# Optimization experiments

Hardware: AMD Instinct MI355X
Metric: run time of the kernel (lower is better)

The kernel has to match this reference:

```python
import jax, jax.numpy as jnp
import numpy as np

V, H, HALF, L, B = 32000, 512, 256, 1024, 64
LN_EPS = 1e-5
DELTA_EPS = 1e-6


def _forward(seq, embed, ff_w1, ff_b1, ff_w2, ff_b2, ln_g, ln_b,
             sem_w, sem_b, epi_w, epi_b, out_w, out_b):
    # Encoder: embed -> residual FFN -> LayerNorm
    e = embed[seq]                                   # (B, L, H)
    ff = jax.nn.relu(e @ ff_w1 + ff_b1) @ ff_w2 + ff_b2
    x = e + ff
    mu = jnp.mean(x, axis=-1, keepdims=True)
    var = jnp.mean((x - mu) ** 2, axis=-1, keepdims=True)
    h = (x - mu) / jnp.sqrt(var + LN_EPS) * ln_g + ln_b  # (B, L, H)

    # Project all timesteps at once (batched GEMM instead of per-step Linear)
    ks_all = h @ sem_w + sem_b                       # (B, L, half)
    ke_all = h @ epi_w + epi_b                       # (B, L, half)

    Bsz = seq.shape[0]
    Ls = seq.shape[1]
    w_t = jnp.arange(1, Ls, dtype=h.dtype) / Ls      # (L-1,) linear recency weights

    def step(carry, inp):
        M_s, M_e = carry
        k_s, k_e, w = inp                            # (B, half), (B, half), scalar
        vps = jnp.einsum('bij,bj->bi', M_s, k_s)
        dvs = k_s - vps / (jnp.sum(k_s * k_s, axis=-1, keepdims=True) + DELTA_EPS)
        M_s = M_s + dvs[:, :, None] * k_s[:, None, :]
        vpe = jnp.einsum('bij,bj->bi', M_e, k_e)
        dve = k_e - vpe / (jnp.sum(k_e * k_e, axis=-1, keepdims=True) + DELTA_EPS)
        M_e = M_e + w * (dve[:, :, None] * k_e[:, None, :])
        return (M_s, M_e), None

    M0 = jnp.zeros((Bsz, HALF, HALF), dtype=h.dtype)
    xs = (jnp.swapaxes(ks_all[:, :-1], 0, 1),        # (L-1, B, half)
          jnp.swapaxes(ke_all[:, :-1], 0, 1),
          w_t)
    (M_s, M_e), _ = jax.lax.scan(step, (M0, M0), xs)

    cs = jnp.einsum('bij,bj->bi', M_s, ks_all[:, -1])
    ce = jnp.einsum('bij,bj->bi', M_e, ke_all[:, -1])
    return jnp.concatenate([cs, ce], axis=-1) @ out_w + out_b  # (B, V)


def setup_inputs() -> dict:
    key = jax.random.key(0)
    ks = jax.random.split(key, 8)
    n = lambda k, shape, s=0.02: jax.random.normal(k, shape, jnp.float32) * s
    return {
        'seq': jax.random.randint(ks[0], (B, L), 0, V),
        'embed': n(ks[1], (V, H)),
        'ff_w1': n(ks[2], (H, 2 * H)), 'ff_b1': jnp.zeros((2 * H,), jnp.float32),
        'ff_w2': n(ks[3], (2 * H, H)), 'ff_b2': jnp.zeros((H,), jnp.float32),
        'ln_g': jnp.ones((H,), jnp.float32), 'ln_b': jnp.zeros((H,), jnp.float32),
        'sem_w': n(ks[4], (H, HALF)), 'sem_b': jnp.zeros((HALF,), jnp.float32),
        'epi_w': n(ks[5], (H, HALF)), 'epi_b': jnp.zeros((HALF,), jnp.float32),
        'out_w': n(ks[6], (2 * HALF, V)), 'out_b': jnp.zeros((V,), jnp.float32),
    }


def reference(seq, embed, ff_w1, ff_b1, ff_w2, ff_b2, ln_g, ln_b,
              sem_w, sem_b, epi_w, epi_b, out_w, out_b):
    return _forward(seq, embed, ff_w1, ff_b1, ff_w2, ff_b2, ln_g, ln_b,
                    sem_w, sem_b, epi_w, epi_b, out_w, out_b)
```

## Files before the change

kernel.cpp:

```cpp
#include <hip/hip_runtime.h>

typedef unsigned short ushort_t;
typedef unsigned int uint_t;
typedef __attribute__((ext_vector_type(8))) short short8;
typedef __attribute__((ext_vector_type(4))) float f32x4;

static constexpr int V = 32000, H = 512, HALFD = 256, LSEQ = 1024, BB = 64;

__device__ __forceinline__ ushort_t f2bf(float f) {
    uint_t u = __float_as_uint(f);
    u = (u + 0x7FFFu + ((u >> 16) & 1u)) >> 16;
    return (ushort_t)u;
}
__device__ __forceinline__ float bf2f(ushort_t u) {
    return __uint_as_float(((uint_t)u) << 16);
}
__device__ __forceinline__ float bflo(uint_t u) { return __uint_as_float(u << 16); }
__device__ __forceinline__ float bfhi(uint_t u) { return __uint_as_float(u & 0xffff0000u); }
__device__ __forceinline__ float bfres(float v) { return v - bf2f(f2bf(v)); }

__device__ __forceinline__ uint_t dppswap1(uint_t x) {
    return (uint_t)__builtin_amdgcn_mov_dpp((int)x, 0xB1, 0xF, 0xF, true);
}

__device__ __forceinline__ void st_pair4(ushort_t* p0, int pitch, int codd,
                                         float v0, float v1, float v2, float v3) {
    uint_t b0 = f2bf(v0), b1 = f2bf(v1), b2 = f2bf(v2), b3 = f2bf(v3);
    uint_t q0 = dppswap1(b0), q1 = dppswap1(b1), q2 = dppswap1(b2), q3 = dppswap1(b3);
    uint_t wa = codd ? ((uint_t)q2 | ((uint_t)b2 << 16)) : ((uint_t)b0 | ((uint_t)q0 << 16));
    uint_t wb = codd ? ((uint_t)q3 | ((uint_t)b3 << 16)) : ((uint_t)b1 | ((uint_t)q1 << 16));
    *(uint_t*)(p0) = wa;
    *(uint_t*)(p0 + pitch) = wb;
}

__global__ void transpose_cvt(const float* __restrict__ W, ushort_t* __restrict__ Wt,
                              int K, int N) {
    __shared__ float tile[32][33];
    int k0 = blockIdx.y * 32, n0 = blockIdx.x * 32;
    int tx = threadIdx.x & 31, ty = threadIdx.x >> 5;
    #pragma unroll
    for (int i = 0; i < 32; i += 8)
        tile[ty + i][tx] = W[(size_t)(k0 + ty + i) * N + n0 + tx];
    __syncthreads();
    #pragma unroll
    for (int i = 0; i < 32; i += 8)
        Wt[(size_t)(n0 + ty + i) * K + k0 + tx] = f2bf(tile[tx][ty + i]);
}

__global__ __launch_bounds__(256) void gemm_ffn1(
        const int* __restrict__ seqp, const float* __restrict__ embed,
        const ushort_t* __restrict__ Bt, const float* __restrict__ bias,
        ushort_t* __restrict__ Cout, int N, int K) {
    __shared__ __align__(16) ushort_t Al[128][40];
    __shared__ __align__(16) ushort_t Bl[128][40];
    int t = threadIdx.x;
    int m0 = blockIdx.y * 128, n0 = blockIdx.x * 128;
    int lane = t & 63, wid = t >> 6;
    int wm = (wid & 1) * 64, wn = (wid >> 1) * 64;
    int lid = lane & 15, quad = lane >> 4;
    int srow = t >> 2, skq = (t & 3) * 8;

    int tok0 = seqp[m0 + srow];
    int tok1 = seqp[m0 + 64 + srow];
    const float* e0 = embed + (size_t)tok0 * H + skq;
    const float* e1 = embed + (size_t)tok1 * H + skq;

    f32x4 acc[4][4];
    #pragma unroll
    for (int i = 0; i < 4; ++i)
        #pragma unroll
        for (int j = 0; j < 4; ++j)
            acc[i][j] = (f32x4){0.f, 0.f, 0.f, 0.f};

    for (int k0 = 0; k0 < K; k0 += 32) {
        float4 ea0 = *(const float4*)(e0 + k0);
        float4 eb0 = *(const float4*)(e0 + k0 + 4);
        float4 ea1 = *(const float4*)(e1 + k0);
        float4 eb1 = *(const float4*)(e1 + k0 + 4);
        short8 b0 = *(const short8*)(Bt + (size_t)(n0 + srow) * K + k0 + skq);
        short8 b1 = *(const short8*)(Bt + (size_t)(n0 + 64 + srow) * K + k0 + skq);
        short8 s0, s1;
        s0[0] = (short)f2bf(ea0.x); s0[1] = (short)f2bf(ea0.y);
        s0[2] = (short)f2bf(ea0.z); s0[3] = (short)f2bf(ea0.w);
        s0[4] = (short)f2bf(eb0.x); s0[5] = (short)f2bf(eb0.y);
        s0[6] = (short)f2bf(eb0.z); s0[7] = (short)f2bf(eb0.w);
        s1[0] = (short)f2bf(ea1.x); s1[1] = (short)f2bf(ea1.y);
        s1[2] = (short)f2bf(ea1.z); s1[3] = (short)f2bf(ea1.w);
        s1[4] = (short)f2bf(eb1.x); s1[5] = (short)f2bf(eb1.y);
        s1[6] = (short)f2bf(eb1.z); s1[7] = (short)f2bf(eb1.w);
        __syncthreads();
        *(short8*)&Al[srow][skq]      = s0;
        *(short8*)&Al[64 + srow][skq] = s1;
        *(short8*)&Bl[srow][skq]      = b0;
        *(short8*)&Bl[64 + srow][skq] = b1;
        __syncthreads();
        short8 af[4], bfr[4];
        #pragma unroll
        for (int i = 0; i < 4; ++i)
            af[i] = *(const short8*)&Al[wm + i * 16 + lid][quad * 8];
        #pragma unroll
        for (int i = 0; i < 4; ++i)
            bfr[i] = *(const short8*)&Bl[wn + i * 16 + lid][quad * 8];
        #pragma unroll
        for (int mt = 0; mt < 4; ++mt)
            #pragma unroll
            for (int nt = 0; nt < 4; ++nt)
                acc[mt][nt] = __builtin_amdgcn_mfma_f32_16x16x32_bf16(
                    af[mt], bfr[nt], acc[mt][nt], 0, 0, 0);
    }
    #pragma unroll
    for (int mt = 0; mt < 4; ++mt)
        #pragma unroll
        for (int nt = 0; nt < 4; ++nt)
            #pragma unroll
            for (int rg = 0; rg < 4; ++rg) {
                int row = m0 + wm + mt * 16 + quad * 4 + rg;
                int col = n0 + wn + nt * 16 + lid;
                float v = fmaxf(acc[mt][nt][rg] + bias[col], 0.f);
                Cout[(size_t)row * N + col] = f2bf(v);
            }
}

__global__ __launch_bounds__(256) void gemm_ffn2(
        const ushort_t* __restrict__ A, const ushort_t* __restrict__ Bt,
        const float* __restrict__ bias, const int* __restrict__ seqp,
        const float* __restrict__ embed, ushort_t* __restrict__ Cout,
        int N, int K) {
    __shared__ __align__(16) ushort_t Al[128][40];
    __shared__ __align__(16) ushort_t Bl[128][40];
    int t = threadIdx.x;
    int m0 = blockIdx.y * 128, n0 = blockIdx.x * 128;
    int lane = t & 63, wid = t >> 6;
    int wm = (wid & 1) * 64, wn = (wid >> 1) * 64;
    int lid = lane & 15, quad = lane >> 4;
    int srow = t >> 2, skq = (t & 3) * 8;

    f32x4 acc[4][4];
    #pragma unroll
    for (int i = 0; i < 4; ++i)
        #pragma unroll
        for (int j = 0; j < 4; ++j)
            acc[i][j] = (f32x4){0.f, 0.f, 0.f, 0.f};

    for (int k0 = 0; k0 < K; k0 += 32) {
        short8 a0 = *(const short8*)(A + (size_t)(m0 + srow) * K + k0 + skq);
        short8 a1 = *(const short8*)(A + (size_t)(m0 + 64 + srow) * K + k0 + skq);
        short8 b0 = *(const short8*)(Bt + (size_t)(n0 + srow) * K + k0 + skq);
        short8 b1 = *(const short8*)(Bt + (size_t)(n0 + 64 + srow) * K + k0 + skq);
        __syncthreads();
        *(short8*)&Al[srow][skq]      = a0;
        *(short8*)&Al[64 + srow][skq] = a1;
        *(short8*)&Bl[srow][skq]      = b0;
        *(short8*)&Bl[64 + srow][skq] = b1;
        __syncthreads();
        short8 af[4], bfr[4];
        #pragma unroll
        for (int i = 0; i < 4; ++i)
            af[i] = *(const short8*)&Al[wm + i * 16 + lid][quad * 8];
        #pragma unroll
        for (int i = 0; i < 4; ++i)
            bfr[i] = *(const short8*)&Bl[wn + i * 16 + lid][quad * 8];
        #pragma unroll
        for (int mt = 0; mt < 4; ++mt)
            #pragma unroll
            for (int nt = 0; nt < 4; ++nt)
                acc[mt][nt] = __builtin_amdgcn_mfma_f32_16x16x32_bf16(
                    af[mt], bfr[nt], acc[mt][nt], 0, 0, 0);
    }
    #pragma unroll
    for (int mt = 0; mt < 4; ++mt)
        #pragma unroll
        for (int rg = 0; rg < 4; ++rg) {
            int row = m0 + wm + mt * 16 + quad * 4 + rg;
            int tok = seqp[row];
            const float* erow = embed + (size_t)tok * H;
            #pragma unroll
            for (int nt = 0; nt < 4; ++nt) {
                int col = n0 + wn + nt * 16 + lid;
                float v = acc[mt][nt][rg] + bias[col] + erow[col];
                Cout[(size_t)row * N + col] = f2bf(v);
            }
        }
}

__global__ __launch_bounds__(256) void gemm_proj(
        const ushort_t* __restrict__ A, const ushort_t* __restrict__ Bt,
        const float* __restrict__ biasS, const float* __restrict__ biasE,
        ushort_t* __restrict__ outS, ushort_t* __restrict__ outE, int K) {
    __shared__ __align__(16) ushort_t Al[128][40];
    __shared__ __align__(16) ushort_t Bl[128][40];
    int t = threadIdx.x;
    int m0 = blockIdx.y * 128, n0 = blockIdx.x * 128;
    int lane = t & 63, wid = t >> 6;
    int wm = (wid & 1) * 64, wn = (wid >> 1) * 64;
    int lid = lane & 15, quad = lane >> 4;
    int srow = t >> 2, skq = (t & 3) * 8;

    f32x4 acc[4][4];
    #pragma unroll
    for (int i = 0; i < 4; ++i)
        #pragma unroll
        for (int j = 0; j < 4; ++j)
            acc[i][j] = (f32x4){0.f, 0.f, 0.f, 0.f};

    for (int k0 = 0; k0 < K; k0 += 32) {
        short8 a0 = *(const short8*)(A + (size_t)(m0 + srow) * K + k0 + skq);
        short8 a1 = *(const short8*)(A + (size_t)(m0 + 64 + srow) * K + k0 + skq);
        short8 b0 = *(const short8*)(Bt + (size_t)(n0 + srow) * K + k0 + skq);
        short8 b1 = *(const short8*)(Bt + (size_t)(n0 + 64 + srow) * K + k0 + skq);
        __syncthreads();
        *(short8*)&Al[srow][skq]      = a0;
        *(short8*)&Al[64 + srow][skq] = a1;
        *(short8*)&Bl[srow][skq]      = b0;
        *(short8*)&Bl[64 + srow][skq] = b1;
        __syncthreads();
        short8 af[4], bfr[4];
        #pragma unroll
        for (int i = 0; i < 4; ++i)
            af[i] = *(const short8*)&Al[wm + i * 16 + lid][quad * 8];
        #pragma unroll
        for (int i = 0; i < 4; ++i)
            bfr[i] = *(const short8*)&Bl[wn + i * 16 + lid][quad * 8];
        #pragma unroll
        for (int mt = 0; mt < 4; ++mt)
            #pragma unroll
            for (int nt = 0; nt < 4; ++nt)
                acc[mt][nt] = __builtin_amdgcn_mfma_f32_16x16x32_bf16(
                    af[mt], bfr[nt], acc[mt][nt], 0, 0, 0);
    }
    #pragma unroll
    for (int mt = 0; mt < 4; ++mt)
        #pragma unroll
        for (int nt = 0; nt < 4; ++nt)
            #pragma unroll
            for (int rg = 0; rg < 4; ++rg) {
                int row = m0 + wm + mt * 16 + quad * 4 + rg;
                int col = n0 + wn + nt * 16 + lid;
                if (col < 256)
                    outS[(size_t)row * HALFD + col] = f2bf(acc[mt][nt][rg] + biasS[col]);
                else
                    outE[(size_t)row * HALFD + col - 256] =
                        f2bf(acc[mt][nt][rg] + biasE[col - 256]);
            }
}

__global__ void ln_kernel(ushort_t* X, const float* __restrict__ g,
                          const float* __restrict__ bta) {
    int row = blockIdx.x * 4 + (threadIdx.x >> 6);
    int lane = threadIdx.x & 63;
    ushort_t* xr = X + (size_t)row * H + lane * 8;
    short8 xv = *(short8*)xr;
    float x[8];
    #pragma unroll
    for (int j = 0; j < 8; ++j) x[j] = bf2f((ushort_t)xv[j]);
    float s = 0.f, ss = 0.f;
    #pragma unroll
    for (int j = 0; j < 8; ++j) { s += x[j]; ss += x[j] * x[j]; }
    #pragma unroll
    for (int d = 1; d < 64; d <<= 1) { s += __shfl_xor(s, d); ss += __shfl_xor(ss, d); }
    float mu = s * (1.f / 512.f);
    float var = ss * (1.f / 512.f) - mu * mu;
    float rstd = rsqrtf(var + 1e-5f);
    float4 g0 = *(const float4*)(g + lane * 8);
    float4 g1 = *(const float4*)(g + lane * 8 + 4);
    float4 b0 = *(const float4*)(bta + lane * 8);
    float4 b1 = *(const float4*)(bta + lane * 8 + 4);
    float gg[8] = {g0.x, g0.y, g0.z, g0.w, g1.x, g1.y, g1.z, g1.w};
    float bb[8] = {b0.x, b0.y, b0.z, b0.w, b1.x, b1.y, b1.z, b1.w};
    short8 o;
    #pragma unroll
    for (int j = 0; j < 8; ++j)
        o[j] = (short)f2bf((x[j] - mu) * rstd * gg[j] + bb[j]);
    *(short8*)xr = o;
}

__global__ void beta_kernel(const ushort_t* __restrict__ k, float* __restrict__ beta) {
    int row = blockIdx.x * 4 + (threadIdx.x >> 6);
    int lane = threadIdx.x & 63;
    ushort4 a = *(const ushort4*)(k + (size_t)row * HALFD + lane * 4);
    float ax = bf2f(a.x), ay = bf2f(a.y), az = bf2f(a.z), aw = bf2f(a.w);
    float s = ax * ax + ay * ay + az * az + aw * aw;
    #pragma unroll
    for (int d = 1; d < 64; d <<= 1) s += __shfl_xor(s, d);
    if (lane == 0) beta[row] = s + 1e-6f;
}

__global__ __launch_bounds__(256) void tinv_kernel(
        const ushort_t* __restrict__ ks, const ushort_t* __restrict__ ke,
        const float* __restrict__ beta_s, const float* __restrict__ beta_e,
        ushort_t* __restrict__ Dg) {
    __shared__ __align__(16) ushort_t Kl[64][280];
    __shared__ __align__(16) ushort_t LmT[4][64][66];
    __shared__ float betsl[4][64];

    int t = threadIdx.x;
    int lane = t & 63, wv = t >> 6;
    int lid = lane & 15, quad = lane >> 4;
    int blk0 = blockIdx.x * 4;
    const float invL = 1.0f / 1024.0f;

    for (int pp = 0; pp < 4; ++pp) {
        int p = blk0 + pp;
        int ch = p & 15, bm = p >> 4;
        int mat = bm & 1, b = bm >> 1;
        const ushort_t* Kp = (mat ? ke : ks) + ((size_t)b * LSEQ + ch * 64) * HALFD;
        const float* Bp = (mat ? beta_e : beta_s) + (size_t)b * LSEQ + ch * 64;

        __syncthreads();
        {
            int j = t >> 2, c0 = (t & 3) * 64;
            const ushort_t* src = Kp + (size_t)j * HALFD + c0;
            #pragma unroll
            for (int x = 0; x < 8; ++x)
                *(short8*)&Kl[j][c0 + x * 8] = *(const short8*)(src + x * 8);
        }
        if (t < 64) betsl[pp][t] = Bp[t];
        __syncthreads();

        f32x4 g[4];
        #pragma unroll
        for (int i = 0; i < 4; ++i) g[i] = (f32x4){0.f, 0.f, 0.f, 0.f};
        #pragma unroll
        for (int kc = 0; kc < 8; ++kc) {
            short8 af = *(const short8*)&Kl[wv * 16 + lid][kc * 32 + quad * 8];
            #pragma unroll
            for (int nt = 0; nt < 4; ++nt) {
                short8 bq = *(const short8*)&Kl[nt * 16 + lid][kc * 32 + quad * 8];
                g[nt] = __builtin_amdgcn_mfma_f32_16x16x32_bf16(af, bq, g[nt], 0, 0, 0);
            }
        }
        #pragma unroll
        for (int nt = 0; nt < 4; ++nt)
            #pragma unroll
            for (int rg = 0; rg < 4; ++rg) {
                int i = wv * 16 + quad * 4 + rg;
                int j = nt * 16 + lid;
                int s = ch * 64 + i;
                float wgt = mat ? (float)(s + 1) * invL : 1.0f;
                if (s >= 1023) wgt = 0.f;
                float wb = wgt / betsl[pp][i];
                LmT[pp][j][i] = f2bf((j < i) ? g[nt][rg] * wb : 0.f);
            }
    }
    __syncthreads();

    const ushort_t (*Lp)[66] = LmT[wv];
    float a[64];
    #pragma unroll
    for (int x = 0; x < 32; ++x) {
        uint_t u = *(const uint_t*)&Lp[lane][x * 2];
        a[x * 2]     = -bflo(u);
        a[x * 2 + 1] = -bfhi(u);
    }
    #pragma unroll
    for (int j = 0; j < 63; ++j) {
        float dj = a[j];
        const ushort_t* rowj = Lp[j];
        #pragma unroll
        for (int ii = (j + 1) & ~1; ii < 64; ii += 2) {
            uint_t u = *(const uint_t*)&rowj[ii];
            if (ii > j) a[ii] -= bflo(u) * dj;
            a[ii + 1]        -= bfhi(u) * dj;
        }
    }
    size_t pbase = (size_t)(blk0 + wv) * 4096;
    #pragma unroll
    for (int i = 0; i < 64; ++i)
        Dg[pbase + (size_t)i * 64 + lane] = f2bf(a[i]);
}

__global__ __launch_bounds__(512) void scan_kernel(
        const ushort_t* __restrict__ ks, const ushort_t* __restrict__ ke,
        const float* __restrict__ beta_s, const float* __restrict__ beta_e,
        const ushort_t* __restrict__ Dg, float* __restrict__ c) {
    int blk = blockIdx.x;
    int b = blk >> 2, mat = (blk >> 1) & 1, half = blk & 1;
    const ushort_t* Kp = (mat ? ke : ks) + (size_t)b * LSEQ * HALFD;
    const float* Bp = (mat ? beta_e : beta_s) + (size_t)b * LSEQ;
    const ushort_t* Dp = Dg + (size_t)(b * 2 + mat) * 16 * 4096;

    __shared__ __align__(16) ushort_t Kl[64][280];
    __shared__ __align__(16) ushort_t MK[35840];
    __shared__ __align__(16) ushort_t RHSl[128][88];
    __shared__ __align__(16) ushort_t Ul[128][88];
    __shared__ __align__(16) ushort_t Dl[64][72];
    __shared__ float betc[64];

    ushort_t (*Ml)[280] = (ushort_t(*)[280])MK;
    ushort_t (*Kt)[88]  = (ushort_t(*)[88])MK;

    int t = threadIdx.x;
    int lane = t & 63, wid = t >> 6;
    int lid = lane & 15, quad = lane >> 4;
    int codd = lid & 1, lid2 = lid & ~1;
    int wm  = (wid & 1) * 64, wn  = (wid >> 1) * 64;
    int wm1 = (wid & 1) * 64, wn1 = (wid >> 1) * 16;

    f32x4 acc[4][4];
    #pragma unroll
    for (int i = 0; i < 4; ++i)
        #pragma unroll
        for (int j = 0; j < 4; ++j)
            acc[i][j] = (f32x4){0.f, 0.f, 0.f, 0.f};

    int sj = t >> 3, scb = (t & 7) * 8;
    short8 pf[4];
    {
        const ushort_t* kr = Kp + (size_t)sj * HALFD + scb;
        #pragma unroll
        for (int x = 0; x < 4; ++x) pf[x] = *(const short8*)(kr + x * 64);
    }
    short8 dpf = *(const short8*)(Dp + t * 8);
    float bpf = (t < 64) ? Bp[t] : 0.f;
    const float invL = 1.0f / 1024.0f;

    for (int ch = 0; ch < 16; ++ch) {
        __syncthreads();
        #pragma unroll
        for (int x = 0; x < 4; ++x) *(short8*)&Kl[sj][scb + x * 64] = pf[x];
        *(short8*)&Dl[t >> 3][(t & 7) * 8] = dpf;
        if (t < 64) betc[t] = bpf;
        #pragma unroll
        for (int mt = 0; mt < 4; ++mt) {
            int rb = wm + mt * 16 + quad * 4 + codd * 2;
            #pragma unroll
            for (int nt = 0; nt < 4; ++nt)
                st_pair4(&Ml[rb][wn + nt * 16 + lid2], 280, codd,
                         acc[mt][nt][0], acc[mt][nt][1], acc[mt][nt][2], acc[mt][nt][3]);
        }
        int nch = (ch + 1 < 16) ? ch + 1 : 15;
        {
            const ushort_t* kr = Kp + ((size_t)nch * 64 + sj) * HALFD + scb;
            #pragma unroll
            for (int x = 0; x < 4; ++x) pf[x] = *(const short8*)(kr + x * 64);
            dpf = *(const short8*)(Dp + (size_t)nch * 4096 + t * 8);
            if (t < 64) bpf = Bp[nch * 64 + t];
        }
        __syncthreads();

        f32x4 p0[4];
        #pragma unroll
        for (int i = 0; i < 4; ++i) p0[i] = (f32x4){0.f, 0.f, 0.f, 0.f};
        #pragma unroll
        for (int kc = 0; kc < 8; ++kc) {
            short8 bq = *(const short8*)&Kl[wn1 + lid][kc * 32 + quad * 8];
            #pragma unroll
            for (int mt = 0; mt < 4; ++mt) {
                short8 aq = *(const short8*)&Ml[wm1 + mt * 16 + lid][kc * 32 + quad * 8];
                p0[mt] = __builtin_amdgcn_mfma_f32_16x16x32_bf16(aq, bq, p0[mt], 0, 0, 0);
            }
        }
        __syncthreads();
        #pragma unroll
        for (int mt = 0; mt < 4; ++mt) {
            int rb = wm + mt * 16 + quad * 4 + codd * 2;
            #pragma unroll
            for (int nt = 0; nt < 4; ++nt)
                st_pair4(&Ml[rb][wn + nt * 16 + lid2], 280, codd,
                         bfres(acc[mt][nt][0]), bfres(acc[mt][nt][1]),
                         bfres(acc[mt][nt][2]), bfres(acc[mt][nt][3]));
        }
        __syncthreads();
        #pragma unroll
        for (int kc = 0; kc < 8; ++kc) {
            short8 bq = *(const short8*)&Kl[wn1 + lid][kc * 32 + quad * 8];
            #pragma unroll
            for (int mt = 0; mt < 4; ++mt) {
                short8 aq = *(const short8*)&Ml[wm1 + mt * 16 + lid][kc * 32 + quad * 8];
                p0[mt] = __builtin_amdgcn_mfma_f32_16x16x32_bf16(aq, bq, p0[mt], 0, 0, 0);
            }
        }
        int iB = wn1 + lid;
        int s = ch * 64 + iB;
        float wgt = mat ? (float)(s + 1) * invL : 1.0f;
        if (s >= 1023) wgt = 0.f;
        float wb = wgt / betc[iB];
        float rhsf[4][4];
        #pragma unroll
        for (int mt = 0; mt < 4; ++mt)
            #pragma unroll
            for (int rg = 0; rg < 4; ++rg) {
                int r = wm1 + mt * 16 + quad * 4 + rg;
                float kv = bf2f(Kl[iB][half * 128 + r]);
                rhsf[mt][rg] = wgt * kv - wb * p0[mt][rg];
            }
        #pragma unroll
        for (int mt = 0; mt < 4; ++mt)
            st_pair4(&RHSl[wm1 + mt * 16 + quad * 4 + codd * 2][wn1 + lid2], 88, codd,
                     rhsf[mt][0], rhsf[mt][1], rhsf[mt][2], rhsf[mt][3]);
        __syncthreads();

        {
            int c0 = wid * 32;
            #pragma unroll
            for (int rr = 0; rr < 4; ++rr) {
                short8 kv8 = *(const short8*)&Kl[lane][c0 + rr * 8];
                #pragma unroll
                for (int x = 0; x < 8; ++x)
                    Kt[c0 + rr * 8 + x][lane] = (ushort_t)kv8[x];
            }
        }
        f32x4 uf[4];
        #pragma unroll
        for (int i = 0; i < 4; ++i) uf[i] = (f32x4){0.f, 0.f, 0.f, 0.f};
        #pragma unroll
        for (int kc = 0; kc < 2; ++kc) {
            short8 bq = *(const short8*)&Dl[wn1 + lid][kc * 32 + quad * 8];
            #pragma unroll
            for (int mt = 0; mt < 4; ++mt) {
                short8 aq = *(const short8*)&RHSl[wm1 + mt * 16 + lid][kc * 32 + quad * 8];
                uf[mt] = __builtin_amdgcn_mfma_f32_16x16x32_bf16(aq, bq, uf[mt], 0, 0, 0);
            }
        }
        #pragma unroll
        for (int mt = 0; mt < 4; ++mt)
            st_pair4(&Ul[wm1 + mt * 16 + quad * 4 + codd * 2][wn1 + lid2], 88, codd,
                     uf[mt][0] + rhsf[mt][0], uf[mt][1] + rhsf[mt][1],
                     uf[mt][2] + rhsf[mt][2], uf[mt][3] + rhsf[mt][3]);
        __syncthreads();
        #pragma unroll
        for (int kc = 0; kc < 2; ++kc) {
            short8 bq4[4];
            #pragma unroll
            for (int nt = 0; nt < 4; ++nt)
                bq4[nt] = *(const short8*)&Kt[wn + nt * 16 + lid][kc * 32 + quad * 8];
            #pragma unroll
            for (int mt = 0; mt < 4; ++mt) {
                short8 aq = *(const short8*)&Ul[wm + mt * 16 + lid][kc * 32 + quad * 8];
                #pragma unroll
                for (int nt = 0; nt < 4; ++nt)
                    acc[mt][nt] = __builtin_amdgcn_mfma_f32_16x16x32_bf16(
                        aq, bq4[nt], acc[mt][nt], 0, 0, 0);
            }
        }
        __syncthreads();
        #pragma unroll
        for (int mt = 0; mt < 4; ++mt) {
            float u0 = uf[mt][0] + rhsf[mt][0], u1 = uf[mt][1] + rhsf[mt][1];
            float u2 = uf[mt][2] + rhsf[mt][2], u3 = uf[mt][3] + rhsf[mt][3];
            st_pair4(&Ul[wm1 + mt * 16 + quad * 4 + codd * 2][wn1 + lid2], 88, codd,
                     bfres(u0), bfres(u1), bfres(u2), bfres(u3));
        }
        __syncthreads();
        #pragma unroll
        for (int kc = 0; kc < 2; ++kc) {
            short8 bq4[4];
            #pragma unroll
            for (int nt = 0; nt < 4; ++nt)
                bq4[nt] = *(const short8*)&Kt[wn + nt * 16 + lid][kc * 32 + quad * 8];
            #pragma unroll
            for (int mt = 0; mt < 4; ++mt) {
                short8 aq = *(const short8*)&Ul[wm + mt * 16 + lid][kc * 32 + quad * 8];
                #pragma unroll
                for (int nt = 0; nt < 4; ++nt)
                    acc[mt][nt] = __builtin_amdgcn_mfma_f32_16x16x32_bf16(
                        aq, bq4[nt], acc[mt][nt], 0, 0, 0);
            }
        }
    }

    __syncthreads();
    float* vsc = (float*)RHSl;
    float kvv[4];
    #pragma unroll
    for (int nt = 0; nt < 4; ++nt)
        kvv[nt] = bf2f(Kl[63][wn + nt * 16 + lid]);
    #pragma unroll
    for (int mt = 0; mt < 4; ++mt)
        #pragma unroll
        for (int rg = 0; rg < 4; ++rg) {
            float p = acc[mt][0][rg] * kvv[0] + acc[mt][1][rg] * kvv[1]
                    + acc[mt][2][rg] * kvv[2] + acc[mt][3][rg] * kvv[3];
            p += __shfl_xor(p, 1); p += __shfl_xor(p, 2);
            p += __shfl_xor(p, 4); p += __shfl_xor(p, 8);
            if (lid == 0)
                vsc[(wid >> 1) * 128 + wm + mt * 16 + quad * 4 + rg] = p;
        }
    __syncthreads();
    if (t < 128) {
        float sum = vsc[t] + vsc[128 + t] + vsc[256 + t] + vsc[384 + t];
        c[(size_t)b * 512 + mat * 256 + half * 128 + t] = sum;
    }
}

__global__ __launch_bounds__(512) void out_gemm(
        const float* __restrict__ c, const float* __restrict__ W,
        const float* __restrict__ bias, float* __restrict__ out) {
    __shared__ __align__(16) float cl[16][512];
    int t = threadIdx.x;
    int lane = t & 63, w = t >> 6;
    int cb = blockIdx.x * 256;
    int rb = blockIdx.y * 16;

    #pragma unroll
    for (int i = 0; i < 4; ++i) {
        int idx = t + i * 512;
        int row = idx >> 7, c4 = (idx & 127) * 4;
        *(float4*)&cl[row][c4] = *(const float4*)(c + (size_t)(rb + row) * 512 + c4);
    }
    __syncthreads();

    const float* wp = W + cb + lane * 4;
    int r0 = w * 2;
    f32x4 a0 = (f32x4){0.f, 0.f, 0.f, 0.f};
    f32x4 a1 = (f32x4){0.f, 0.f, 0.f, 0.f};

    #pragma unroll 2
    for (int k = 0; k < 512; k += 4) {
        f32x4 w0 = *(const f32x4*)(wp + (size_t)(k + 0) * V);
        f32x4 w1 = *(const f32x4*)(wp + (size_t)(k + 1) * V);
        f32x4 w2 = *(const f32x4*)(wp + (size_t)(k + 2) * V);
        f32x4 w3 = *(const f32x4*)(wp + (size_t)(k + 3) * V);
        f32x4 ca = *(const f32x4*)&cl[r0][k];
        f32x4 cb4 = *(const f32x4*)&cl[r0 + 1][k];
        a0 += ca[0] * w0; a0 += ca[1] * w1; a0 += ca[2] * w2; a0 += ca[3] * w3;
        a1 += cb4[0] * w0; a1 += cb4[1] * w1; a1 += cb4[2] * w2; a1 += cb4[3] * w3;
    }
    f32x4 bv = *(const f32x4*)(bias + cb + lane * 4);
    *(f32x4*)(out + (size_t)(rb + r0) * V + cb + lane * 4) = a0 + bv;
    *(f32x4*)(out + (size_t)(rb + r0 + 1) * V + cb + lane * 4) = a1 + bv;
}

extern "C" void kernel_launch(void* const* d_in, const int* in_sizes, int n_in,
                              void* d_out, int out_size, void* d_ws, size_t ws_size,
                              hipStream_t stream) {
    const int*   seq    = (const int*)d_in[0];
    const float* embed  = (const float*)d_in[1];
    const float* ff_w1  = (const float*)d_in[2];
    const float* ff_b1  = (const float*)d_in[3];
    const float* ff_w2  = (const float*)d_in[4];
    const float* ff_b2  = (const float*)d_in[5];
    const float* ln_g   = (const float*)d_in[6];
    const float* ln_b   = (const float*)d_in[7];
    const float* sem_w  = (const float*)d_in[8];
    const float* sem_b  = (const float*)d_in[9];
    const float* epi_w  = (const float*)d_in[10];
    const float* epi_b  = (const float*)d_in[11];
    const float* out_w  = (const float*)d_in[12];
    const float* out_b  = (const float*)d_in[13];
    float* outp = (float*)d_out;

    const int ML = BB * LSEQ;
    int RCH;
    if      (ws_size >= 271712256ull) RCH = 65536;
    else if (ws_size >= 120717312ull) RCH = 16384;
    else                              RCH = 8192;

    char* w = (char*)d_ws;
    size_t off = 0;
    ushort_t* ks_bf = (ushort_t*)(w + off); off += 33554432;
    ushort_t* ke_bf = (ushort_t*)(w + off); off += 33554432;
    ushort_t* ebc   = (ushort_t*)(w + off); off += (size_t)RCH * 512 * 2;
    ushort_t* t1c   = (ushort_t*)(w + off); off += (size_t)RCH * 1024 * 2;
    ushort_t* w1t   = (ushort_t*)(w + off); off += 1048576;
    ushort_t* w2t   = (ushort_t*)(w + off); off += 1048576;
    ushort_t* semt  = (ushort_t*)(w + off); off += 262144;
    ushort_t* epit  = (ushort_t*)(w + off); off += 262144;
    float*    bet_s = (float*)(w + off);    off += 262144;
    float*    bet_e = (float*)(w + off);    off += 262144;
    float*    cbuf  = (float*)(w + off);    off += 131072;
    ushort_t* Dbuf  = ebc;
    (void)t1c;

    transpose_cvt<<<dim3(1024 / 32, 512 / 32), 256, 0, stream>>>(ff_w1, w1t, 512, 1024);
    transpose_cvt<<<dim3(512 / 32, 1024 / 32), 256, 0, stream>>>(ff_w2, w2t, 1024, 512);
    transpose_cvt<<<dim3(256 / 32, 512 / 32), 256, 0, stream>>>(sem_w, semt, 512, 256);
    transpose_cvt<<<dim3(256 / 32, 512 / 32), 256, 0, stream>>>(epi_w, epit, 512, 256);

    for (int cc = 0; cc < ML / RCH; ++cc) {
        int c0 = cc * RCH;
        gemm_ffn1<<<dim3(1024 / 128, RCH / 128), 256, 0, stream>>>(
            seq + c0, embed, w1t, ff_b1, t1c, 1024, 512);
        gemm_ffn2<<<dim3(512 / 128, RCH / 128), 256, 0, stream>>>(
            t1c, w2t, ff_b2, seq + c0, embed, ebc, 512, 1024);
        ln_kernel<<<RCH / 4, 256, 0, stream>>>(ebc, ln_g, ln_b);
        gemm_proj<<<dim3(512 / 128, RCH / 128), 256, 0, stream>>>(
            ebc, semt, sem_b, epi_b,
            ks_bf + (size_t)c0 * HALFD, ke_bf + (size_t)c0 * HALFD, 512);
    }

    beta_kernel<<<ML / 4, 256, 0, stream>>>(ks_bf, bet_s);
    beta_kernel<<<ML / 4, 256, 0, stream>>>(ke_bf, bet_e);

    tinv_kernel<<<512, 256, 0, stream>>>(ks_bf, ke_bf, bet_s, bet_e, Dbuf);
    scan_kernel<<<256, 512, 0, stream>>>(ks_bf, ke_bf, bet_s, bet_e, Dbuf, cbuf);

    out_gemm<<<dim3(125, 4), 512, 0, stream>>>(cbuf, out_w, out_b, outp);
}
```

Measured before the change: 961.9 us.

## Use direct global-to-LDS loads and XOR-swizzled LDS layouts in GEMMs and scan

The projection GEMMs now stage tiles with global_load_lds (direct global-to-LDS DMA) into unpadded, XOR-swizzled LDS buffers instead of loading through registers and storing into padded arrays. The chunked delta-rule scan kernel replaces its padded LDS arrays and DPP-paired bf16 stores with swizzled layouts and plain per-element 16-bit stores. The aim is to cut bank conflicts, register staging and LDS footprint. In exchange it adds more scalar 2-byte LDS writes in the scan and depends on the swizzle keys matching exactly between writers and readers.

```diff
diff --git a/kernel.cpp b/kernel.cpp
--- a/kernel.cpp
+++ b/kernel.cpp
@@ -19,18 +19,24 @@
 __device__ __forceinline__ float bfhi(uint_t u) { return __uint_as_float(u & 0xffff0000u); }
 __device__ __forceinline__ float bfres(float v) { return v - bf2f(f2bf(v)); }
 
-__device__ __forceinline__ uint_t dppswap1(uint_t x) {
-    return (uint_t)__builtin_amdgcn_mov_dpp((int)x, 0xB1, 0xF, 0xF, true);
-}
-
-__device__ __forceinline__ void st_pair4(ushort_t* p0, int pitch, int codd,
-                                         float v0, float v1, float v2, float v3) {
-    uint_t b0 = f2bf(v0), b1 = f2bf(v1), b2 = f2bf(v2), b3 = f2bf(v3);
-    uint_t q0 = dppswap1(b0), q1 = dppswap1(b1), q2 = dppswap1(b2), q3 = dppswap1(b3);
-    uint_t wa = codd ? ((uint_t)q2 | ((uint_t)b2 << 16)) : ((uint_t)b0 | ((uint_t)q0 << 16));
-    uint_t wb = codd ? ((uint_t)q3 | ((uint_t)b3 << 16)) : ((uint_t)b1 | ((uint_t)q1 << 16));
-    *(uint_t*)(p0) = wa;
-    *(uint_t*)(p0 + pitch) = wb;
+typedef const __attribute__((address_space(1))) void* gas_ptr;
+typedef __attribute__((address_space(3))) void* las_ptr;
+#define GLDS16(g, l) __builtin_amdgcn_global_load_lds((gas_ptr)(g), (las_ptr)(l), 16, 0, 0)
+
+__device__ __forceinline__ const short8* rd64(const ushort_t* b, int row, int chunk) {
+    return (const short8*)(b + row * 32 + (((chunk ^ ((row >> 1) & 3)) & 3) << 3));
+}
+__device__ __forceinline__ ushort_t* wr64(ushort_t* b, int row, int chunk) {
+    return b + row * 32 + (((chunk ^ ((row >> 1) & 3)) & 3) << 3);
+}
+
+__device__ __forceinline__ int swz512(int row, int colbyte) {
+    int key = (((row & 7) ^ ((row >> 2) & 7)) & 7) << 4;
+    return row * 256 + ((colbyte ^ key) >> 1);
+}
+__device__ __forceinline__ int swz128(int row, int colbyte) {
+    int key = (((row & 7) ^ ((row >> 2) & 7)) & 7) << 4;
+    return row * 64 + ((colbyte ^ key) >> 1);
 }
 
 __global__ void transpose_cvt(const float* __restrict__ W, ushort_t* __restrict__ Wt,
@@ -51,19 +57,24 @@
         const int* __restrict__ seqp, const float* __restrict__ embed,
         const ushort_t* __restrict__ Bt, const float* __restrict__ bias,
         ushort_t* __restrict__ Cout, int N, int K) {
-    __shared__ __align__(16) ushort_t Al[128][40];
-    __shared__ __align__(16) ushort_t Bl[128][40];
+    __shared__ __align__(16) ushort_t Al[4096];
+    __shared__ __align__(16) ushort_t Bl[4096];
     int t = threadIdx.x;
     int m0 = blockIdx.y * 128, n0 = blockIdx.x * 128;
     int lane = t & 63, wid = t >> 6;
     int wm = (wid & 1) * 64, wn = (wid >> 1) * 64;
     int lid = lane & 15, quad = lane >> 4;
-    int srow = t >> 2, skq = (t & 3) * 8;
+    int srow = t >> 2;
+    int gch = (t & 3) ^ ((t >> 3) & 3);
 
     int tok0 = seqp[m0 + srow];
     int tok1 = seqp[m0 + 64 + srow];
-    const float* e0 = embed + (size_t)tok0 * H + skq;
-    const float* e1 = embed + (size_t)tok1 * H + skq;
+    const float* e0 = embed + (size_t)tok0 * H + (t & 3) * 8;
+    const float* e1 = embed + (size_t)tok1 * H + (t & 3) * 8;
+    const ushort_t* b0p = Bt + (size_t)(n0 + srow) * K + gch * 8;
+    const ushort_t* b1p = Bt + (size_t)(n0 + 64 + srow) * K + gch * 8;
+    ushort_t* ldsB = Bl + wid * 512;
+    ushort_t* aw0 = wr64(Al, srow, t & 3);
 
     f32x4 acc[4][4];
     #pragma unroll
@@ -73,12 +84,13 @@
             acc[i][j] = (f32x4){0.f, 0.f, 0.f, 0.f};
 
     for (int k0 = 0; k0 < K; k0 += 32) {
+        __syncthreads();
+        GLDS16(b0p + k0, ldsB);
+        GLDS16(b1p + k0, ldsB + 2048);
         float4 ea0 = *(const float4*)(e0 + k0);
         float4 eb0 = *(const float4*)(e0 + k0 + 4);
         float4 ea1 = *(const float4*)(e1 + k0);
         float4 eb1 = *(const float4*)(e1 + k0 + 4);
-        short8 b0 = *(const short8*)(Bt + (size_t)(n0 + srow) * K + k0 + skq);
-        short8 b1 = *(const short8*)(Bt + (size_t)(n0 + 64 + srow) * K + k0 + skq);
         short8 s0, s1;
         s0[0] = (short)f2bf(ea0.x); s0[1] = (short)f2bf(ea0.y);
         s0[2] = (short)f2bf(ea0.z); s0[3] = (short)f2bf(ea0.w);
@@ -88,19 +100,14 @@
         s1[2] = (short)f2bf(ea1.z); s1[3] = (short)f2bf(ea1.w);
         s1[4] = (short)f2bf(eb1.x); s1[5] = (short)f2bf(eb1.y);
         s1[6] = (short)f2bf(eb1.z); s1[7] = (short)f2bf(eb1.w);
-        __syncthreads();
-        *(short8*)&Al[srow][skq]      = s0;
-        *(short8*)&Al[64 + srow][skq] = s1;
-        *(short8*)&Bl[srow][skq]      = b0;
-        *(short8*)&Bl[64 + srow][skq] = b1;
+        *(short8*)aw0 = s0;
+        *(short8*)(aw0 + 2048) = s1;
         __syncthreads();
         short8 af[4], bfr[4];
         #pragma unroll
-        for (int i = 0; i < 4; ++i)
-            af[i] = *(const short8*)&Al[wm + i * 16 + lid][quad * 8];
-        #pragma unroll
-        for (int i = 0; i < 4; ++i)
-            bfr[i] = *(const short8*)&Bl[wn + i * 16 + lid][quad * 8];
+        for (int i = 0; i < 4; ++i) af[i] = *rd64(Al, wm + i * 16 + lid, quad);
+        #pragma unroll
+        for (int i = 0; i < 4; ++i) bfr[i] = *rd64(Bl, wn + i * 16 + lid, quad);
         #pragma unroll
         for (int mt = 0; mt < 4; ++mt)
             #pragma unroll
@@ -126,14 +133,22 @@
         const float* __restrict__ bias, const int* __restrict__ seqp,
         const float* __restrict__ embed, ushort_t* __restrict__ Cout,
         int N, int K) {
-    __shared__ __align__(16) ushort_t Al[128][40];
-    __shared__ __align__(16) ushort_t Bl[128][40];
+    __shared__ __align__(16) ushort_t Al[4096];
+    __shared__ __align__(16) ushort_t Bl[4096];
     int t = threadIdx.x;
     int m0 = blockIdx.y * 128, n0 = blockIdx.x * 128;
     int lane = t & 63, wid = t >> 6;
     int wm = (wid & 1) * 64, wn = (wid >> 1) * 64;
     int lid = lane & 15, quad = lane >> 4;
-    int srow = t >> 2, skq = (t & 3) * 8;
+    int srow = t >> 2;
+    int gch = (t & 3) ^ ((t >> 3) & 3);
+
+    const ushort_t* a0p = A + (size_t)(m0 + srow) * K + gch * 8;
+    const ushort_t* a1p = A + (size_t)(m0 + 64 + srow) * K + gch * 8;
+    const ushort_t* b0p = Bt + (size_t)(n0 + srow) * K + gch * 8;
+    const ushort_t* b1p = Bt + (size_t)(n0 + 64 + srow) * K + gch * 8;
+    ushort_t* ldsA = Al + wid * 512;
+    ushort_t* ldsB = Bl + wid * 512;
 
     f32x4 acc[4][4];
     #pragma unroll
@@ -143,23 +158,17 @@
             acc[i][j] = (f32x4){0.f, 0.f, 0.f, 0.f};
 
     for (int k0 = 0; k0 < K; k0 += 32) {
-        short8 a0 = *(const short8*)(A + (size_t)(m0 + srow) * K + k0 + skq);
-        short8 a1 = *(const short8*)(A + (size_t)(m0 + 64 + srow) * K + k0 + skq);
-        short8 b0 = *(const short8*)(Bt + (size_t)(n0 + srow) * K + k0 + skq);
-        short8 b1 = *(const short8*)(Bt + (size_t)(n0 + 64 + srow) * K + k0 + skq);
-        __syncthreads();
-        *(short8*)&Al[srow][skq]      = a0;
-        *(short8*)&Al[64 + srow][skq] = a1;
-        *(short8*)&Bl[srow][skq]      = b0;
-        *(short8*)&Bl[64 + srow][skq] = b1;
+        __syncthreads();
+        GLDS16(a0p + k0, ldsA);
+        GLDS16(a1p + k0, ldsA + 2048);
+        GLDS16(b0p + k0, ldsB);
+        GLDS16(b1p + k0, ldsB + 2048);
         __syncthreads();
         short8 af[4], bfr[4];
         #pragma unroll
-        for (int i = 0; i < 4; ++i)
-            af[i] = *(const short8*)&Al[wm + i * 16 + lid][quad * 8];
-        #pragma unroll
-        for (int i = 0; i < 4; ++i)
-            bfr[i] = *(const short8*)&Bl[wn + i * 16 + lid][quad * 8];
+        for (int i = 0; i < 4; ++i) af[i] = *rd64(Al, wm + i * 16 + lid, quad);
+        #pragma unroll
+        for (int i = 0; i < 4; ++i) bfr[i] = *rd64(Bl, wn + i * 16 + lid, quad);
         #pragma unroll
         for (int mt = 0; mt < 4; ++mt)
             #pragma unroll
@@ -187,14 +196,22 @@
         const ushort_t* __restrict__ A, const ushort_t* __restrict__ Bt,
         const float* __restrict__ biasS, const float* __restrict__ biasE,
         ushort_t* __restrict__ outS, ushort_t* __restrict__ outE, int K) {
-    __shared__ __align__(16) ushort_t Al[128][40];
-    __shared__ __align__(16) ushort_t Bl[128][40];
+    __shared__ __align__(16) ushort_t Al[4096];
+    __shared__ __align__(16) ushort_t Bl[4096];
     int t = threadIdx.x;
     int m0 = blockIdx.y * 128, n0 = blockIdx.x * 128;
     int lane = t & 63, wid = t >> 6;
     int wm = (wid & 1) * 64, wn = (wid >> 1) * 64;
     int lid = lane & 15, quad = lane >> 4;
-    int srow = t >> 2, skq = (t & 3) * 8;
+    int srow = t >> 2;
+    int gch = (t & 3) ^ ((t >> 3) & 3);
+
+    const ushort_t* a0p = A + (size_t)(m0 + srow) * K + gch * 8;
+    const ushort_t* a1p = A + (size_t)(m0 + 64 + srow) * K + gch * 8;
+    const ushort_t* b0p = Bt + (size_t)(n0 + srow) * K + gch * 8;
+    const ushort_t* b1p = Bt + (size_t)(n0 + 64 + srow) * K + gch * 8;
+    ushort_t* ldsA = Al + wid * 512;
+    ushort_t* ldsB = Bl + wid * 512;
 
     f32x4 acc[4][4];
     #pragma unroll
@@ -204,23 +221,17 @@
             acc[i][j] = (f32x4){0.f, 0.f, 0.f, 0.f};
 
     for (int k0 = 0; k0 < K; k0 += 32) {
-        short8 a0 = *(const short8*)(A + (size_t)(m0 + srow) * K + k0 + skq);
-        short8 a1 = *(const short8*)(A + (size_t)(m0 + 64 + srow) * K + k0 + skq);
-        short8 b0 = *(const short8*)(Bt + (size_t)(n0 + srow) * K + k0 + skq);
-        short8 b1 = *(const short8*)(Bt + (size_t)(n0 + 64 + srow) * K + k0 + skq);
-        __syncthreads();
-        *(short8*)&Al[srow][skq]      = a0;
-        *(short8*)&Al[64 + srow][skq] = a1;
-        *(short8*)&Bl[srow][skq]      = b0;
-        *(short8*)&Bl[64 + srow][skq] = b1;
+        __syncthreads();
+        GLDS16(a0p + k0, ldsA);
+        GLDS16(a1p + k0, ldsA + 2048);
+        GLDS16(b0p + k0, ldsB);
+        GLDS16(b1p + k0, ldsB + 2048);
         __syncthreads();
         short8 af[4], bfr[4];
         #pragma unroll
-        for (int i = 0; i < 4; ++i)
-            af[i] = *(const short8*)&Al[wm + i * 16 + lid][quad * 8];
-        #pragma unroll
-        for (int i = 0; i < 4; ++i)
-            bfr[i] = *(const short8*)&Bl[wn + i * 16 + lid][quad * 8];
+        for (int i = 0; i < 4; ++i) af[i] = *rd64(Al, wm + i * 16 + lid, quad);
+        #pragma unroll
+        for (int i = 0; i < 4; ++i) bfr[i] = *rd64(Bl, wn + i * 16 + lid, quad);
         #pragma unroll
         for (int mt = 0; mt < 4; ++mt)
             #pragma unroll
@@ -379,20 +390,16 @@
     const float* Bp = (mat ? beta_e : beta_s) + (size_t)b * LSEQ;
     const ushort_t* Dp = Dg + (size_t)(b * 2 + mat) * 16 * 4096;
 
-    __shared__ __align__(16) ushort_t Kl[64][280];
-    __shared__ __align__(16) ushort_t MK[35840];
-    __shared__ __align__(16) ushort_t RHSl[128][88];
-    __shared__ __align__(16) ushort_t Ul[128][88];
+    __shared__ __align__(16) ushort_t Kl[16384];
+    __shared__ __align__(16) ushort_t MK[32768];
+    __shared__ __align__(16) ushort_t RHSl[8192];
+    __shared__ __align__(16) ushort_t Ul[8192];
     __shared__ __align__(16) ushort_t Dl[64][72];
     __shared__ float betc[64];
-
-    ushort_t (*Ml)[280] = (ushort_t(*)[280])MK;
-    ushort_t (*Kt)[88]  = (ushort_t(*)[88])MK;
 
     int t = threadIdx.x;
     int lane = t & 63, wid = t >> 6;
     int lid = lane & 15, quad = lane >> 4;
-    int codd = lid & 1, lid2 = lid & ~1;
     int wm  = (wid & 1) * 64, wn  = (wid >> 1) * 64;
     int wm1 = (wid & 1) * 64, wn1 = (wid >> 1) * 16;
 
@@ -403,10 +410,10 @@
         for (int j = 0; j < 4; ++j)
             acc[i][j] = (f32x4){0.f, 0.f, 0.f, 0.f};
 
-    int sj = t >> 3, scb = (t & 7) * 8;
+    int sj = t >> 3, scb = (t & 7) * 16;
     short8 pf[4];
     {
-        const ushort_t* kr = Kp + (size_t)sj * HALFD + scb;
+        const ushort_t* kr = Kp + (size_t)sj * HALFD + (t & 7) * 8;
         #pragma unroll
         for (int x = 0; x < 4; ++x) pf[x] = *(const short8*)(kr + x * 64);
     }
@@ -417,20 +424,21 @@
     for (int ch = 0; ch < 16; ++ch) {
         __syncthreads();
         #pragma unroll
-        for (int x = 0; x < 4; ++x) *(short8*)&Kl[sj][scb + x * 64] = pf[x];
+        for (int x = 0; x < 4; ++x)
+            *(short8*)&Kl[swz512(sj, scb + x * 128)] = pf[x];
         *(short8*)&Dl[t >> 3][(t & 7) * 8] = dpf;
         if (t < 64) betc[t] = bpf;
         #pragma unroll
-        for (int mt = 0; mt < 4; ++mt) {
-            int rb = wm + mt * 16 + quad * 4 + codd * 2;
+        for (int mt = 0; mt < 4; ++mt)
             #pragma unroll
             for (int nt = 0; nt < 4; ++nt)
-                st_pair4(&Ml[rb][wn + nt * 16 + lid2], 280, codd,
-                         acc[mt][nt][0], acc[mt][nt][1], acc[mt][nt][2], acc[mt][nt][3]);
-        }
+                #pragma unroll
+                for (int rg = 0; rg < 4; ++rg)
+                    MK[swz512(wm + mt * 16 + quad * 4 + rg, (wn + nt * 16 + lid) * 2)] =
+                        f2bf(acc[mt][nt][rg]);
         int nch = (ch + 1 < 16) ? ch + 1 : 15;
         {
-            const ushort_t* kr = Kp + ((size_t)nch * 64 + sj) * HALFD + scb;
+            const ushort_t* kr = Kp + ((size_t)nch * 64 + sj) * HALFD + (t & 7) * 8;
             #pragma unroll
             for (int x = 0; x < 4; ++x) pf[x] = *(const short8*)(kr + x * 64);
             dpf = *(const short8*)(Dp + (size_t)nch * 4096 + t * 8);
@@ -443,30 +451,31 @@
         for (int i = 0; i < 4; ++i) p0[i] = (f32x4){0.f, 0.f, 0.f, 0.f};
         #pragma unroll
         for (int kc = 0; kc < 8; ++kc) {
-            short8 bq = *(const short8*)&Kl[wn1 + lid][kc * 32 + quad * 8];
+            short8 bq = *(const short8*)&Kl[swz512(wn1 + lid, kc * 64 + quad * 16)];
             #pragma unroll
             for (int mt = 0; mt < 4; ++mt) {
-                short8 aq = *(const short8*)&Ml[wm1 + mt * 16 + lid][kc * 32 + quad * 8];
+                short8 aq = *(const short8*)&MK[swz512(wm1 + mt * 16 + lid,
+                                                       kc * 64 + quad * 16)];
                 p0[mt] = __builtin_amdgcn_mfma_f32_16x16x32_bf16(aq, bq, p0[mt], 0, 0, 0);
             }
         }
         __syncthreads();
         #pragma unroll
-        for (int mt = 0; mt < 4; ++mt) {
-            int rb = wm + mt * 16 + quad * 4 + codd * 2;
+        for (int mt = 0; mt < 4; ++mt)
             #pragma unroll
             for (int nt = 0; nt < 4; ++nt)
-                st_pair4(&Ml[rb][wn + nt * 16 + lid2], 280, codd,
-                         bfres(acc[mt][nt][0]), bfres(acc[mt][nt][1]),
-                         bfres(acc[mt][nt][2]), bfres(acc[mt][nt][3]));
-        }
+                #pragma unroll
+                for (int rg = 0; rg < 4; ++rg)
+                    MK[swz512(wm + mt * 16 + quad * 4 + rg, (wn + nt * 16 + lid) * 2)] =
+                        f2bf(bfres(acc[mt][nt][rg]));
         __syncthreads();
         #pragma unroll
         for (int kc = 0; kc < 8; ++kc) {
-            short8 bq = *(const short8*)&Kl[wn1 + lid][kc * 32 + quad * 8];
+            short8 bq = *(const short8*)&Kl[swz512(wn1 + lid, kc * 64 + quad * 16)];
             #pragma unroll
             for (int mt = 0; mt < 4; ++mt) {
-                short8 aq = *(const short8*)&Ml[wm1 + mt * 16 + lid][kc * 32 + quad * 8];
+                short8 aq = *(const short8*)&MK[swz512(wm1 + mt * 16 + lid,
+                                                       kc * 64 + quad * 16)];
                 p0[mt] = __builtin_amdgcn_mfma_f32_16x16x32_bf16(aq, bq, p0[mt], 0, 0, 0);
             }
         }
@@ -481,23 +490,21 @@
             #pragma unroll
             for (int rg = 0; rg < 4; ++rg) {
                 int r = wm1 + mt * 16 + quad * 4 + rg;
-                float kv = bf2f(Kl[iB][half * 128 + r]);
-                rhsf[mt][rg] = wgt * kv - wb * p0[mt][rg];
-            }
-        #pragma unroll
-        for (int mt = 0; mt < 4; ++mt)
-            st_pair4(&RHSl[wm1 + mt * 16 + quad * 4 + codd * 2][wn1 + lid2], 88, codd,
-                     rhsf[mt][0], rhsf[mt][1], rhsf[mt][2], rhsf[mt][3]);
+                float kv = bf2f(Kl[swz512(iB, (half * 128 + r) * 2)]);
+                float rv = wgt * kv - wb * p0[mt][rg];
+                rhsf[mt][rg] = rv;
+                RHSl[swz128(r, iB * 2)] = f2bf(rv);
+            }
         __syncthreads();
 
         {
-            int c0 = wid * 32;
+            int c0b = wid * 64;
             #pragma unroll
             for (int rr = 0; rr < 4; ++rr) {
-                short8 kv8 = *(const short8*)&Kl[lane][c0 + rr * 8];
+                short8 kv8 = *(const short8*)&Kl[swz512(lane, c0b + rr * 16)];
                 #pragma unroll
                 for (int x = 0; x < 8; ++x)
-                    Kt[c0 + rr * 8 + x][lane] = (ushort_t)kv8[x];
+                    MK[swz128(wid * 32 + rr * 8 + x, lane * 2)] = (ushort_t)kv8[x];
             }
         }
         f32x4 uf[4];
@@ -508,25 +515,30 @@
             short8 bq = *(const short8*)&Dl[wn1 + lid][kc * 32 + quad * 8];
             #pragma unroll
             for (int mt = 0; mt < 4; ++mt) {
-                short8 aq = *(const short8*)&RHSl[wm1 + mt * 16 + lid][kc * 32 + quad * 8];
+                short8 aq = *(const short8*)&RHSl[swz128(wm1 + mt * 16 + lid,
+                                                         kc * 64 + quad * 16)];
                 uf[mt] = __builtin_amdgcn_mfma_f32_16x16x32_bf16(aq, bq, uf[mt], 0, 0, 0);
             }
         }
         #pragma unroll
         for (int mt = 0; mt < 4; ++mt)
-            st_pair4(&Ul[wm1 + mt * 16 + quad * 4 + codd * 2][wn1 + lid2], 88, codd,
-                     uf[mt][0] + rhsf[mt][0], uf[mt][1] + rhsf[mt][1],
-                     uf[mt][2] + rhsf[mt][2], uf[mt][3] + rhsf[mt][3]);
+            #pragma unroll
+            for (int rg = 0; rg < 4; ++rg) {
+                int r = wm1 + mt * 16 + quad * 4 + rg;
+                Ul[swz128(r, iB * 2)] = f2bf(uf[mt][rg] + rhsf[mt][rg]);
+            }
         __syncthreads();
         #pragma unroll
         for (int kc = 0; kc < 2; ++kc) {
             short8 bq4[4];
             #pragma unroll
             for (int nt = 0; nt < 4; ++nt)
-                bq4[nt] = *(const short8*)&Kt[wn + nt * 16 + lid][kc * 32 + quad * 8];
+                bq4[nt] = *(const short8*)&MK[swz128(wn + nt * 16 + lid,
+                                                     kc * 64 + quad * 16)];
             #pragma unroll
             for (int mt = 0; mt < 4; ++mt) {
-                short8 aq = *(const short8*)&Ul[wm + mt * 16 + lid][kc * 32 + quad * 8];
+                short8 aq = *(const short8*)&Ul[swz128(wm + mt * 16 + lid,
+                                                       kc * 64 + quad * 16)];
                 #pragma unroll
                 for (int nt = 0; nt < 4; ++nt)
                     acc[mt][nt] = __builtin_amdgcn_mfma_f32_16x16x32_bf16(
@@ -535,22 +547,25 @@
         }
         __syncthreads();
         #pragma unroll
-        for (int mt = 0; mt < 4; ++mt) {
-            float u0 = uf[mt][0] + rhsf[mt][0], u1 = uf[mt][1] + rhsf[mt][1];
-            float u2 = uf[mt][2] + rhsf[mt][2], u3 = uf[mt][3] + rhsf[mt][3];
-            st_pair4(&Ul[wm1 + mt * 16 + quad * 4 + codd * 2][wn1 + lid2], 88, codd,
-                     bfres(u0), bfres(u1), bfres(u2), bfres(u3));
-        }
+        for (int mt = 0; mt < 4; ++mt)
+            #pragma unroll
+            for (int rg = 0; rg < 4; ++rg) {
+                int r = wm1 + mt * 16 + quad * 4 + rg;
+                float u = uf[mt][rg] + rhsf[mt][rg];
+                Ul[swz128(r, iB * 2)] = f2bf(bfres(u));
+            }
         __syncthreads();
         #pragma unroll
         for (int kc = 0; kc < 2; ++kc) {
             short8 bq4[4];
             #pragma unroll
             for (int nt = 0; nt < 4; ++nt)
-                bq4[nt] = *(const short8*)&Kt[wn + nt * 16 + lid][kc * 32 + quad * 8];
+                bq4[nt] = *(const short8*)&MK[swz128(wn + nt * 16 + lid,
+                                                     kc * 64 + quad * 16)];
             #pragma unroll
             for (int mt = 0; mt < 4; ++mt) {
-                short8 aq = *(const short8*)&Ul[wm + mt * 16 + lid][kc * 32 + quad * 8];
+                short8 aq = *(const short8*)&Ul[swz128(wm + mt * 16 + lid,
+                                                       kc * 64 + quad * 16)];
                 #pragma unroll
                 for (int nt = 0; nt < 4; ++nt)
                     acc[mt][nt] = __builtin_amdgcn_mfma_f32_16x16x32_bf16(
@@ -564,7 +579,7 @@
     float kvv[4];
     #pragma unroll
     for (int nt = 0; nt < 4; ++nt)
-        kvv[nt] = bf2f(Kl[63][wn + nt * 16 + lid]);
+        kvv[nt] = bf2f(Kl[swz512(63, (wn + nt * 16 + lid) * 2)]);
     #pragma unroll
     for (int mt = 0; mt < 4; ++mt)
         #pragma unroll
```

After: 1.295 ms. 1.35x slower.
